# Performance work log

Measured on AMD Instinct MI355X. Metric: run time of the kernel, lower is better.

## Reference

```python
import jax, jax.numpy as jnp
import numpy as np

D_MODEL = 1024

def setup_inputs() -> dict:
    key = jax.random.key(0)
    kx, kq, kk, kv, ko = jax.random.split(key, 5)
    B, S, D = 4, 2048, D_MODEL
    scale = 1.0 / np.sqrt(D)
    return {
        "x": jax.random.normal(kx, (B, S, D), dtype=jnp.float32),
        "w_q": jax.random.normal(kq, (D, D), dtype=jnp.float32) * scale,
        "w_k": jax.random.normal(kk, (D, D), dtype=jnp.float32) * scale,
        "w_v": jax.random.normal(kv, (D, D), dtype=jnp.float32) * scale,
        "w_out": jax.random.normal(ko, (D, D), dtype=jnp.float32) * scale,
    }

def reference(x, w_q, w_k, w_v, w_out):
    # Single-head attention: projections are Linear(d_model,d_model,bias=False).
    # torch Linear computes x @ W.T; weights here stored as [out,in].
    Q = jnp.einsum('bsd,ed->bse', x, w_q)
    K = jnp.einsum('bsd,ed->bse', x, w_k)
    V = jnp.einsum('bsd,ed->bse', x, w_v)
    d_model = x.shape[-1]
    scores = jnp.einsum('bqe,bke->bqk', Q, K) / jnp.sqrt(jnp.float32(d_model))
    attn = jax.nn.softmax(scores, axis=-1)
    out = jnp.einsum('bqk,bke->bqe', attn, V)
    return jnp.einsum('bse,oe->bso', out, w_out)
```

## Files before the change

kernel.cpp:

```cpp
#include <hip/hip_runtime.h>

typedef unsigned int uint;
typedef unsigned short ushort;
typedef __bf16 bf16x8 __attribute__((ext_vector_type(8)));
typedef float f32x4 __attribute__((ext_vector_type(4)));

__device__ __forceinline__ ushort f2bf(float v) {
    uint u = __builtin_bit_cast(uint, v);
    u += 0x7fffu + ((u >> 16) & 1u);
    return (ushort)(u >> 16);
}

__device__ __forceinline__ void storeval(float* p, float v)  { *p = v; }
__device__ __forceinline__ void storeval(ushort* p, float v) { *p = f2bf(v); }

#define GLDS(g, l) __builtin_amdgcn_global_load_lds( \
    (const __attribute__((address_space(1))) uint*)(g), \
    (__attribute__((address_space(3))) uint*)(l), 16, 0, 0)

#define VMW(N)  asm volatile("s_waitcnt vmcnt(" #N ")" ::: "memory")
#define SBAR()  asm volatile("s_barrier" ::: "memory")

__device__ __forceinline__ void stage_half(const ushort* __restrict__ src, int ld,
                                           int halfrow, char* ldsbase, int tid)
{
#pragma unroll
    for (int i = 0; i < 2; i++) {
        const int byte = i * 8192 + tid * 16;
        const int row  = byte >> 7;
        const int slot = (byte >> 4) & 7;
        const int srcs = slot ^ (row & 7);
        GLDS(src + (long long)(halfrow + row) * ld + srcs * 8,
             ldsbase + halfrow * 128 + byte);
    }
}

__device__ __forceinline__ bf16x8 ldf(const char* base, int rbase, int ks,
                                      int lrow, int lquad)
{
    const int r    = rbase + lrow;
    const int slot = ((ks << 2) + lquad) ^ (r & 7);
    return *(const bf16x8*)(base + r * 128 + slot * 16);
}

#define RD_A(BASE, ROFF) \
    _Pragma("unroll") for (int m_ = 0; m_ < 4; m_++) \
    _Pragma("unroll") for (int k_ = 0; k_ < 2; k_++) \
        af[m_][k_] = ldf(BASE, (ROFF) + m_ * 16, k_, lrow, lquad);

#define RD_B(DST, BASE, ROFF) \
    _Pragma("unroll") for (int n_ = 0; n_ < 2; n_++) \
    _Pragma("unroll") for (int k_ = 0; k_ < 2; k_++) \
        DST[n_][k_] = ldf(BASE, (ROFF) + n_ * 16, k_, lrow, lquad);

#define QUAD(MOFF, NOFF, B) \
    __builtin_amdgcn_s_setprio(1); \
    _Pragma("unroll") for (int m_ = 0; m_ < 4; m_++) \
    _Pragma("unroll") for (int n_ = 0; n_ < 2; n_++) \
    _Pragma("unroll") for (int k_ = 0; k_ < 2; k_++) \
        acc[(MOFF) + m_][(NOFF) + n_] = __builtin_amdgcn_mfma_f32_16x16x32_bf16( \
            af[m_][k_], B[n_][k_], acc[(MOFF) + m_][(NOFF) + n_], 0, 0, 0); \
    __builtin_amdgcn_s_setprio(0);

template<bool EXP>
__global__ __launch_bounds__(512, 2)
void gemm256_8ph(const ushort* __restrict__ A, int lda, long long bsA,
                 const ushort* __restrict__ Bt, int ldb, long long bsB,
                 ushort* __restrict__ C, int ldc, long long bsC,
                 int K, float scale, float* __restrict__ Zp)
{
    __shared__ char smem[131072];
    char* A0 = smem;
    char* A1 = smem + 32768;
    char* B0 = smem + 65536;
    char* B1 = smem + 98304;

    const int tid   = threadIdx.x;
    const int lane  = tid & 63;
    const int wave  = tid >> 6;
    const int wr    = wave >> 2;
    const int wc    = wave & 3;
    const int lrow  = lane & 15;
    const int lquad = lane >> 4;
    const long long b = blockIdx.z;

    const ushort* Ag = A  + b * bsA + (long long)blockIdx.y * 256 * lda;
    const ushort* Bg = Bt + b * bsB + (long long)blockIdx.x * 256 * ldb;
    ushort*       Cg = C  + b * bsC + (long long)blockIdx.y * 256 * ldc
                           + (long long)blockIdx.x * 256;

    f32x4 acc[8][4] = {};
    bf16x8 af[4][2], bl[2][2], bh[2][2];

    const int nk    = K >> 6;
    const int nIter = nk >> 1;

    stage_half(Ag,      lda, 0,   A0, tid);
    stage_half(Bg,      ldb, 0,   B0, tid);
    stage_half(Bg,      ldb, 128, B0, tid);
    stage_half(Ag,      lda, 128, A0, tid);
    stage_half(Ag + 64, lda, 0,   A1, tid);
    stage_half(Bg + 64, ldb, 0,   B1, tid);
    stage_half(Bg + 64, ldb, 128, B1, tid);
    VMW(6); SBAR();

    for (int i = 0; i < nIter - 1; ++i) {
        const ushort* An1 = Ag + (2 * i + 1) * 64;
        const ushort* An2 = Ag + (2 * i + 2) * 64;
        const ushort* Bn2 = Bg + (2 * i + 2) * 64;
        const ushort* An3 = Ag + (2 * i + 3) * 64;
        const ushort* Bn3 = Bg + (2 * i + 3) * 64;

        RD_A(A0, wr * 64); RD_B(bl, B0, wc * 32);
        stage_half(An1, lda, 128, A1, tid);
        SBAR(); QUAD(0, 0, bl); SBAR();

        RD_B(bh, B0, 128 + wc * 32);
        stage_half(An2, lda, 0, A0, tid);
        SBAR(); QUAD(0, 2, bh); SBAR();

        RD_A(A0, 128 + wr * 64);
        stage_half(Bn2, ldb, 0, B0, tid);
        SBAR(); QUAD(4, 0, bl); SBAR();

        stage_half(Bn2, ldb, 128, B0, tid);
        SBAR(); QUAD(4, 2, bh); VMW(6); SBAR();

        RD_A(A1, wr * 64); RD_B(bl, B1, wc * 32);
        stage_half(An2, lda, 128, A0, tid);
        SBAR(); QUAD(0, 0, bl); SBAR();

        RD_B(bh, B1, 128 + wc * 32);
        stage_half(An3, lda, 0, A1, tid);
        SBAR(); QUAD(0, 2, bh); SBAR();

        RD_A(A1, 128 + wr * 64);
        stage_half(Bn3, ldb, 0, B1, tid);
        SBAR(); QUAD(4, 0, bl); SBAR();

        stage_half(Bn3, ldb, 128, B1, tid);
        SBAR(); QUAD(4, 2, bh); VMW(6); SBAR();
    }

    {
        const ushort* An1 = Ag + (nk - 1) * 64;

        RD_A(A0, wr * 64); RD_B(bl, B0, wc * 32);
        stage_half(An1, lda, 128, A1, tid);
        SBAR(); QUAD(0, 0, bl); SBAR();

        RD_B(bh, B0, 128 + wc * 32);
        SBAR(); QUAD(0, 2, bh); SBAR();

        RD_A(A0, 128 + wr * 64);
        SBAR(); QUAD(4, 0, bl); SBAR();

        SBAR(); QUAD(4, 2, bh); VMW(0); SBAR();

        RD_A(A1, wr * 64); RD_B(bl, B1, wc * 32);
        SBAR(); QUAD(0, 0, bl); SBAR();

        RD_B(bh, B1, 128 + wc * 32);
        SBAR(); QUAD(0, 2, bh); SBAR();

        RD_A(A1, 128 + wr * 64);
        SBAR(); QUAD(4, 0, bl); SBAR();

        SBAR(); QUAD(4, 2, bh);
    }

#pragma unroll
    for (int m = 0; m < 8; m++) {
        const int row = (m >> 2) * 128 + wr * 64 + (m & 3) * 16 + lquad * 4;
        float rs[4] = {0.f, 0.f, 0.f, 0.f};
#pragma unroll
        for (int n = 0; n < 4; n++) {
            const int col = (n >> 1) * 128 + wc * 32 + (n & 1) * 16 + lrow;
#pragma unroll
            for (int j = 0; j < 4; j++) {
                float v = acc[m][n][j];
                if (EXP) {
                    float e = __expf(v * scale);
                    rs[j] += e;
                    Cg[(long long)(row + j) * ldc + col] = f2bf(e);
                } else {
                    Cg[(long long)(row + j) * ldc + col] = f2bf(v);
                }
            }
        }
        if (EXP) {
#pragma unroll
            for (int j = 0; j < 4; j++) {
                float s = rs[j];
                s += __shfl_xor(s, 1);
                s += __shfl_xor(s, 2);
                s += __shfl_xor(s, 4);
                s += __shfl_xor(s, 8);
                rs[j] = s;
            }
            if (lrow == 0) {
                const long long zi = ((long long)b * 32 + blockIdx.x * 4 + wc) * 2048
                                   + (long long)blockIdx.y * 256 + row;
#pragma unroll
                for (int j = 0; j < 4; j++) Zp[zi + j] = rs[j];
            }
        }
    }
}

template<typename OUT_T, bool ZSCALE>
__global__ __launch_bounds__(512, 2)
void gemm_bm128(const ushort* __restrict__ A, int lda, long long bsA,
                const ushort* __restrict__ Bt, int ldb, long long bsB,
                OUT_T* __restrict__ C, int ldc, long long bsC,
                int K, const float* __restrict__ Zp)
{
    __shared__ char smem[98304];
    __shared__ float zbuf[128];

    const int tid   = threadIdx.x;
    const int lane  = tid & 63;
    const int wave  = tid >> 6;
    const int wr    = wave >> 2;
    const int wc    = wave & 3;
    const int lrow  = lane & 15;
    const int lquad = lane >> 4;
    const long long b = blockIdx.z;

    if (ZSCALE) {
        if (tid < 128) {
            const float* p = Zp + b * 32 * 2048
                           + (long long)blockIdx.y * 128 + tid;
            float s = 0.f;
#pragma unroll
            for (int i = 0; i < 32; i++) s += p[i * 2048];
            zbuf[tid] = 1.0f / s;
        }
        __syncthreads();
    }

    const ushort* Ag = A  + b * bsA + (long long)blockIdx.y * 128 * lda;
    const ushort* Bg = Bt + b * bsB + (long long)blockIdx.x * 256 * ldb;
    OUT_T*        Cg = C  + b * bsC + (long long)blockIdx.y * 128 * ldc
                           + (long long)blockIdx.x * 256;

    f32x4 acc[4][4] = {};
    bf16x8 af[4][2], bl[2][2], bh[2][2];

    const int nk = K >> 6;

    stage_half(Ag, lda, 0,   smem,         tid);
    stage_half(Bg, ldb, 0,   smem + 32768, tid);
    stage_half(Bg, ldb, 128, smem + 32768, tid);
    VMW(2); SBAR();

    for (int t = 0; t < nk - 1; ++t) {
        const int cur = t & 1;
        const char* lAc = smem + cur * 16384;
        const char* lBc = smem + 32768 + cur * 32768;
        char* lAn = smem + (cur ^ 1) * 16384;
        char* lBn = smem + 32768 + (cur ^ 1) * 32768;
        const ushort* An = Ag + (t + 1) * 64;
        const ushort* Bn = Bg + (t + 1) * 64;

        RD_A(lAc, wr * 64);
        RD_B(bl, lBc, wc * 32);
        stage_half(An, lda, 0, lAn, tid);
        stage_half(Bn, ldb, 0, lBn, tid);
        SBAR();
        QUAD(0, 0, bl);
        VMW(4); SBAR();

        RD_B(bh, lBc, 128 + wc * 32);
        stage_half(Bn, ldb, 128, lBn, tid);
        SBAR();
        QUAD(0, 2, bh);
        VMW(2); SBAR();
    }

    {
        const int cur = (nk - 1) & 1;
        const char* lAc = smem + cur * 16384;
        const char* lBc = smem + 32768 + cur * 32768;

        RD_A(lAc, wr * 64);
        RD_B(bl, lBc, wc * 32);
        SBAR();
        QUAD(0, 0, bl);
        VMW(0); SBAR();

        RD_B(bh, lBc, 128 + wc * 32);
        SBAR();
        QUAD(0, 2, bh);
    }

#pragma unroll
    for (int m = 0; m < 4; m++) {
        const int row = wr * 64 + m * 16 + lquad * 4;
        f32x4 z4;
        if (ZSCALE) z4 = *(const f32x4*)&zbuf[row];
#pragma unroll
        for (int n = 0; n < 4; n++) {
            const int col = (n >> 1) * 128 + wc * 32 + (n & 1) * 16 + lrow;
#pragma unroll
            for (int j = 0; j < 4; j++) {
                float v = acc[m][n][j];
                if (ZSCALE) v *= z4[j];
                storeval(&Cg[(long long)(row + j) * ldc + col], v);
            }
        }
    }
}

__global__ __launch_bounds__(256)
void wgemm_splitk(const ushort* __restrict__ A0, const ushort* __restrict__ B0,
                  const ushort* __restrict__ A1, const ushort* __restrict__ B1,
                  float* __restrict__ P)
{
    __shared__ ushort lA[128 * 64];
    __shared__ ushort lB[128 * 64];

    const int z    = blockIdx.z;
    const int pair = z >> 1;
    const int ksl  = z & 1;

    const ushort* A  = pair ? A1 : A0;
    const ushort* Bt = pair ? B1 : B0;

    const int tid  = threadIdx.x;
    const int lane = tid & 63;
    const int wave = tid >> 6;
    const int wr   = wave >> 1;
    const int wc   = wave & 1;

    A  += (long long)blockIdx.y * 128 * 1024 + ksl * 512;
    Bt += (long long)blockIdx.x * 128 * 1024 + ksl * 512;
    float* Pg = P + (long long)z * 1048576
                  + (long long)blockIdx.y * 128 * 1024 + (long long)blockIdx.x * 128;

    f32x4 acc[4][4] = {};
    const int byte_base = wave * 1024 + lane * 16;

    for (int kt = 0; kt < 512; kt += 64) {
#pragma unroll
        for (int i = 0; i < 4; i++) {
            const int byte = i * 4096 + byte_base;
            const int row  = byte >> 7;
            const int k0   = (byte & 127) >> 1;
            GLDS(A  + (long long)row * 1024 + kt + k0, (char*)lA + byte);
            GLDS(Bt + (long long)row * 1024 + kt + k0, (char*)lB + byte);
        }
        __syncthreads();

#pragma unroll
        for (int ks = 0; ks < 2; ks++) {
            bf16x8 af2[4], bf2[4];
#pragma unroll
            for (int m = 0; m < 4; m++)
                af2[m] = *(const bf16x8*)&lA[(wr * 64 + m * 16 + (lane & 15)) * 64 + ks * 32 + (lane >> 4) * 8];
#pragma unroll
            for (int n = 0; n < 4; n++)
                bf2[n] = *(const bf16x8*)&lB[(wc * 64 + n * 16 + (lane & 15)) * 64 + ks * 32 + (lane >> 4) * 8];
#pragma unroll
            for (int m = 0; m < 4; m++)
#pragma unroll
                for (int n = 0; n < 4; n++)
                    acc[m][n] = __builtin_amdgcn_mfma_f32_16x16x32_bf16(af2[m], bf2[n], acc[m][n], 0, 0, 0);
        }
        __syncthreads();
    }

    const int r0 = wr * 64 + (lane >> 4) * 4;
    const int c0 = wc * 64 + (lane & 15);
#pragma unroll
    for (int m = 0; m < 4; m++)
#pragma unroll
        for (int n = 0; n < 4; n++)
#pragma unroll
            for (int j = 0; j < 4; j++)
                Pg[(long long)(r0 + m * 16 + j) * 1024 + c0 + n * 16] = acc[m][n][j];
}

__global__ __launch_bounds__(256)
void wreduce(const float* __restrict__ P, ushort* __restrict__ W2)
{
    const int i = blockIdx.x * 256 + threadIdx.x;
    const int pair = i >> 18;
    const int off  = (i & 262143) * 4;
    const float* base = P + (long long)pair * 2097152 + off;
    float4 s = *(const float4*)(base);
    float4 v = *(const float4*)(base + 1048576);
    s.x += v.x; s.y += v.y; s.z += v.z; s.w += v.w;
    ushort o[4] = { f2bf(s.x), f2bf(s.y), f2bf(s.z), f2bf(s.w) };
    *(uint2*)&W2[(long long)pair * 1048576 + off] = *(const uint2*)&o[0];
}

__global__ __launch_bounds__(256)
void f32_to_bf16_vec(const float* __restrict__ in, ushort* __restrict__ out, int n4)
{
    int i = blockIdx.x * 256 + threadIdx.x;
    if (i >= n4) return;
    float4 v = ((const float4*)in)[i];
    ushort o[4] = { f2bf(v.x), f2bf(v.y), f2bf(v.z), f2bf(v.w) };
    *(uint2*)&out[(size_t)i * 4] = *(const uint2*)&o[0];
}

__global__ __launch_bounds__(256)
void wprep(const float* __restrict__ s0, const float* __restrict__ s1,
           const float* __restrict__ s2, const float* __restrict__ s3,
           ushort* __restrict__ wT, ushort* __restrict__ wo_bf)
{
    __shared__ float t[64][65];
    const int z = blockIdx.z;
    const int k0 = blockIdx.y * 64, j0 = blockIdx.x * 64;
    const int r = threadIdx.x >> 2;
    const int c = (threadIdx.x & 3) * 16;

    if (z == 3) {
        const float* p = s3 + (size_t)(k0 + r) * 1024 + j0 + c;
        float4 a = *(const float4*)(p);
        float4 bq = *(const float4*)(p + 4);
        float4 cc = *(const float4*)(p + 8);
        float4 d = *(const float4*)(p + 12);
        ushort o[16] = { f2bf(a.x), f2bf(a.y), f2bf(a.z), f2bf(a.w),
                         f2bf(bq.x), f2bf(bq.y), f2bf(bq.z), f2bf(bq.w),
                         f2bf(cc.x), f2bf(cc.y), f2bf(cc.z), f2bf(cc.w),
                         f2bf(d.x), f2bf(d.y), f2bf(d.z), f2bf(d.w) };
        ushort* q = wo_bf + (size_t)(k0 + r) * 1024 + j0 + c;
        *(uint4*)q       = *(const uint4*)&o[0];
        *(uint4*)(q + 8) = *(const uint4*)&o[8];
        return;
    }

    const float* src = (z == 0) ? s0 : (z == 1) ? s1 : s2;
    ushort* dst = wT + (size_t)z * 1048576;

    const float* p = src + (size_t)(k0 + r) * 1024 + j0 + c;
#pragma unroll
    for (int j = 0; j < 16; j++) t[r][c + j] = p[j];
    __syncthreads();

    ushort o[16];
#pragma unroll
    for (int j = 0; j < 16; j++) o[j] = f2bf(t[c + j][r]);
    ushort* q = dst + (size_t)(j0 + r) * 1024 + k0 + c;
    *(uint4*)q       = *(const uint4*)&o[0];
    *(uint4*)(q + 8) = *(const uint4*)&o[8];
}

__global__ __launch_bounds__(256)
void transpose_v(const ushort* __restrict__ V, int ldv, long long bsV,
                 ushort* __restrict__ Vt)
{
    __shared__ ushort t[64][65];
    const int b = blockIdx.z;
    const ushort* src = V  + (size_t)b * bsV;
    ushort*       dst = Vt + (size_t)b * 1024 * 2048;
    const int e0 = blockIdx.x * 64;
    const int k0 = blockIdx.y * 64;
    const int r = threadIdx.x >> 2;
    const int c = (threadIdx.x & 3) * 16;

    const ushort* p = &src[(size_t)(k0 + r) * ldv + e0 + c];
    ushort vals[16];
    *(uint4*)&vals[0] = *(const uint4*)p;
    *(uint4*)&vals[8] = *(const uint4*)(p + 8);
#pragma unroll
    for (int j = 0; j < 16; j++) t[r][c + j] = vals[j];
    __syncthreads();

    ushort o[16];
#pragma unroll
    for (int j = 0; j < 16; j++) o[j] = t[c + j][r];
    ushort* q = &dst[(size_t)(e0 + r) * 2048 + k0 + c];
    *(uint4*)q       = *(const uint4*)&o[0];
    *(uint4*)(q + 8) = *(const uint4*)&o[8];
}

extern "C" void kernel_launch(void* const* d_in, const int* in_sizes, int n_in,
                              void* d_out, int out_size, void* d_ws, size_t ws_size,
                              hipStream_t stream)
{
    const float* x  = (const float*)d_in[0];
    const float* wq = (const float*)d_in[1];
    const float* wk = (const float*)d_in[2];
    const float* wv = (const float*)d_in[3];
    const float* wo = (const float*)d_in[4];
    float* out = (float*)d_out;

    char* ws = (char*)d_ws;
    ushort* xb    = (ushort*)(ws);
    ushort* W2    = (ushort*)(ws + 16777216);
    ushort* wT    = (ushort*)(ws + 20971520);
    ushort* wo_bf = (ushort*)(ws + 27262976);
    ushort* TVw   = (ushort*)(ws + 29360128);
    ushort* Vtb   = (ushort*)(ws + 62914560);
    ushort* E     = (ushort*)(ws + 79691776);
    float*  Pp    = (float*)(ws + 79691776);
    float*  Zp    = (float*)(ws + 113246208);

    ushort* wqT = wT;
    ushort* wkT = wT + 1048576;
    ushort* wvT = wT + 2097152;

    f32_to_bf16_vec<<<8192, 256, 0, stream>>>(x, xb, 2097152);
    wprep<<<dim3(16, 16, 4), 256, 0, stream>>>(wq, wk, wv, wo, wT, wo_bf);

    wgemm_splitk<<<dim3(8, 8, 4), 256, 0, stream>>>(wkT, wqT, wo_bf, wvT, Pp);
    wreduce<<<2048, 256, 0, stream>>>(Pp, W2);

    gemm256_8ph<false><<<dim3(8, 32, 1), 512, 0, stream>>>(
        xb, 1024, 0, W2, 1024, 0, TVw, 2048, 0, 1024, 1.f, nullptr);

    transpose_v<<<dim3(16, 32, 4), 256, 0, stream>>>(TVw + 1024, 2048, 2048LL * 2048, Vtb);

    gemm256_8ph<true><<<dim3(8, 8, 4), 512, 0, stream>>>(
        TVw, 2048, 2048LL * 2048, xb, 1024, 2048LL * 1024,
        E, 2048, 2048LL * 2048, 1024, 0.03125f, Zp);

    gemm_bm128<float, true><<<dim3(4, 16, 4), 512, 0, stream>>>(
        E, 2048, 2048LL * 2048, Vtb, 2048, 1024LL * 2048,
        out, 1024, 2048LL * 1024, 2048, Zp);
}
```

Baseline: 164.5 us.

## Triple-buffer LDS in PV GEMM with one barrier per k-step

Replaces the templated double-buffered bm128 GEMM used for the attention-times-V product with a dedicated kernel that keeps three LDS stages and prefetches two tiles ahead. Each k-step now reads all A and B fragments up front, issues the next-next tile load, runs both MFMA quads, then does a single wait and barrier instead of four barriers per step. The goal is to hide global-to-LDS latency better and cut synchronisation stalls. The cost is LDS growing to 144KB, which caps residency at one block per CU and holds more fragments in registers at once.

```diff
diff --git a/kernel.cpp b/kernel.cpp
--- a/kernel.cpp
+++ b/kernel.cpp
@@ -208,14 +208,13 @@
     }
 }
 
-template<typename OUT_T, bool ZSCALE>
 __global__ __launch_bounds__(512, 2)
-void gemm_bm128(const ushort* __restrict__ A, int lda, long long bsA,
-                const ushort* __restrict__ Bt, int ldb, long long bsB,
-                OUT_T* __restrict__ C, int ldc, long long bsC,
-                int K, const float* __restrict__ Zp)
-{
-    __shared__ char smem[98304];
+void pv3(const ushort* __restrict__ A, int lda, long long bsA,
+         const ushort* __restrict__ Bt, int ldb, long long bsB,
+         float* __restrict__ C, int ldc, long long bsC,
+         int K, const float* __restrict__ Zp)
+{
+    __shared__ char smem[147456];
     __shared__ float zbuf[128];
 
     const int tid   = threadIdx.x;
@@ -227,21 +226,18 @@
     const int lquad = lane >> 4;
     const long long b = blockIdx.z;
 
-    if (ZSCALE) {
-        if (tid < 128) {
-            const float* p = Zp + b * 32 * 2048
-                           + (long long)blockIdx.y * 128 + tid;
-            float s = 0.f;
-#pragma unroll
-            for (int i = 0; i < 32; i++) s += p[i * 2048];
-            zbuf[tid] = 1.0f / s;
-        }
-        __syncthreads();
-    }
+    if (tid < 128) {
+        const float* p = Zp + b * 32 * 2048 + (long long)blockIdx.y * 128 + tid;
+        float s = 0.f;
+#pragma unroll
+        for (int i = 0; i < 32; i++) s += p[i * 2048];
+        zbuf[tid] = 1.0f / s;
+    }
+    __syncthreads();
 
     const ushort* Ag = A  + b * bsA + (long long)blockIdx.y * 128 * lda;
     const ushort* Bg = Bt + b * bsB + (long long)blockIdx.x * 256 * ldb;
-    OUT_T*        Cg = C  + b * bsC + (long long)blockIdx.y * 128 * ldc
+    float*        Cg = C  + b * bsC + (long long)blockIdx.y * 128 * ldc
                            + (long long)blockIdx.x * 256;
 
     f32x4 acc[4][4] = {};
@@ -249,65 +245,51 @@
 
     const int nk = K >> 6;
 
-    stage_half(Ag, lda, 0,   smem,         tid);
-    stage_half(Bg, ldb, 0,   smem + 32768, tid);
-    stage_half(Bg, ldb, 128, smem + 32768, tid);
-    VMW(2); SBAR();
-
-    for (int t = 0; t < nk - 1; ++t) {
-        const int cur = t & 1;
+#define STAGE_TILE(T, I) do { \
+        stage_half(Ag + (T) * 64, lda, 0,   smem + (I) * 16384,         tid); \
+        stage_half(Bg + (T) * 64, ldb, 0,   smem + 49152 + (I) * 32768, tid); \
+        stage_half(Bg + (T) * 64, ldb, 128, smem + 49152 + (I) * 32768, tid); \
+    } while (0)
+
+    STAGE_TILE(0, 0);
+    STAGE_TILE(1, 1);
+    VMW(6); SBAR();
+
+    int cur = 0;
+    for (int t = 0; t < nk; ++t) {
         const char* lAc = smem + cur * 16384;
-        const char* lBc = smem + 32768 + cur * 32768;
-        char* lAn = smem + (cur ^ 1) * 16384;
-        char* lBn = smem + 32768 + (cur ^ 1) * 32768;
-        const ushort* An = Ag + (t + 1) * 64;
-        const ushort* Bn = Bg + (t + 1) * 64;
+        const char* lBc = smem + 49152 + cur * 32768;
 
         RD_A(lAc, wr * 64);
         RD_B(bl, lBc, wc * 32);
-        stage_half(An, lda, 0, lAn, tid);
-        stage_half(Bn, ldb, 0, lBn, tid);
-        SBAR();
+        RD_B(bh, lBc, 128 + wc * 32);
+
+        if (t + 2 < nk) {
+            int nxt = cur + 2; if (nxt >= 3) nxt -= 3;
+            STAGE_TILE(t + 2, nxt);
+        }
+
         QUAD(0, 0, bl);
-        VMW(4); SBAR();
-
-        RD_B(bh, lBc, 128 + wc * 32);
-        stage_half(Bn, ldb, 128, lBn, tid);
-        SBAR();
         QUAD(0, 2, bh);
-        VMW(2); SBAR();
-    }
-
-    {
-        const int cur = (nk - 1) & 1;
-        const char* lAc = smem + cur * 16384;
-        const char* lBc = smem + 32768 + cur * 32768;
-
-        RD_A(lAc, wr * 64);
-        RD_B(bl, lBc, wc * 32);
-        SBAR();
-        QUAD(0, 0, bl);
-        VMW(0); SBAR();
-
-        RD_B(bh, lBc, 128 + wc * 32);
-        SBAR();
-        QUAD(0, 2, bh);
-    }
+
+        if (t + 1 < nk) {
+            if (t + 2 < nk) { VMW(6); } else { VMW(0); }
+            SBAR();
+        }
+        cur = (cur == 2) ? 0 : cur + 1;
+    }
+#undef STAGE_TILE
 
 #pragma unroll
     for (int m = 0; m < 4; m++) {
         const int row = wr * 64 + m * 16 + lquad * 4;
-        f32x4 z4;
-        if (ZSCALE) z4 = *(const f32x4*)&zbuf[row];
+        f32x4 z4 = *(const f32x4*)&zbuf[row];
 #pragma unroll
         for (int n = 0; n < 4; n++) {
             const int col = (n >> 1) * 128 + wc * 32 + (n & 1) * 16 + lrow;
 #pragma unroll
-            for (int j = 0; j < 4; j++) {
-                float v = acc[m][n][j];
-                if (ZSCALE) v *= z4[j];
-                storeval(&Cg[(long long)(row + j) * ldc + col], v);
-            }
+            for (int j = 0; j < 4; j++)
+                storeval(&Cg[(long long)(row + j) * ldc + col], acc[m][n][j] * z4[j]);
         }
     }
 }
@@ -518,7 +500,7 @@
         TVw, 2048, 2048LL * 2048, xb, 1024, 2048LL * 1024,
         E, 2048, 2048LL * 2048, 1024, 0.03125f, Zp);
 
-    gemm_bm128<float, true><<<dim3(4, 16, 4), 512, 0, stream>>>(
+    pv3<<<dim3(4, 16, 4), 512, 0, stream>>>(
         E, 2048, 2048LL * 2048, Vtb, 2048, 1024LL * 2048,
         out, 1024, 2048LL * 1024, 2048, Zp);
 }
```

Measured after the change: 164.5 us. Within noise of the previous version (-0.0%).
